# Kernel tuning notes

Hardware: AMD Instinct MI355X
Metric: run time of the kernel (lower is better)

The kernel has to match this reference:

```python
import jax, jax.numpy as jnp
import numpy as np
import math

H = 16
D_MODEL = 1024
D_K = D_MODEL // H


def setup_inputs() -> dict:
    key = jax.random.key(0)
    ks = jax.random.split(key, 11)
    B, S, D = 4, 2048, D_MODEL
    scale = 1.0 / math.sqrt(D)
    inp = {
        "query": jax.random.normal(ks[0], (B, S, D), jnp.float32),
        "key": jax.random.normal(ks[1], (B, S, D), jnp.float32),
        "value": jax.random.normal(ks[2], (B, S, D), jnp.float32),
        # four Linear(d_model, d_model) layers: Wq, Wk, Wv, Wo (weights stored [in, out])
        "Wq": jax.random.normal(ks[3], (D, D), jnp.float32) * scale,
        "bq": jnp.zeros((D,), jnp.float32),
        "Wk": jax.random.normal(ks[4], (D, D), jnp.float32) * scale,
        "bk": jnp.zeros((D,), jnp.float32),
        "Wv": jax.random.normal(ks[5], (D, D), jnp.float32) * scale,
        "bv": jnp.zeros((D,), jnp.float32),
        "Wo": jax.random.normal(ks[6], (D, D), jnp.float32) * scale,
        "bo": jnp.zeros((D,), jnp.float32),
    }
    return inp


def reference(query, key, value, Wq, bq, Wk, bk, Wv, bv, Wo, bo):
    B, S, D = query.shape
    # QKV projections, split into heads: [B, H, S, d_k]
    def proj(x, W, b):
        return (x @ W + b).reshape(B, -1, H, D_K).transpose(0, 2, 1, 3)

    q = proj(query, Wq, bq)
    k = proj(key, Wk, bk)
    v = proj(value, Wv, bv)

    # scaled dot-product attention (mask=None, dropout p=0 -> identity)
    scores = jnp.einsum("bhqd,bhkd->bhqk", q, k) / math.sqrt(D_K)
    p_attn = jax.nn.softmax(scores, axis=-1)
    x = jnp.einsum("bhqk,bhkd->bhqd", p_attn, v)

    # merge heads and output projection
    x = x.transpose(0, 2, 1, 3).reshape(B, -1, H * D_K)
    return x @ Wo + bo
```

## Files before the change

### kernel.cpp

```cpp
#include <hip/hip_runtime.h>


typedef unsigned short u16;
typedef unsigned int u32;
typedef __attribute__((ext_vector_type(8))) short bfx8;
typedef __attribute__((ext_vector_type(4))) float f32x4;
typedef __attribute__((ext_vector_type(16))) float f32x16;
typedef __attribute__((ext_vector_type(4))) float fx4;
typedef __attribute__((ext_vector_type(8))) u16 u16x8;
typedef __attribute__((ext_vector_type(4))) u16 u16x4;
typedef __attribute__((ext_vector_type(4))) u32 u32x4;

__device__ __forceinline__ u16 f2bf(float f) {
  union { float f; u32 u; } v; v.f = f;
  u32 u = v.u;
  u += 0x7fffu + ((u >> 16) & 1u);
  return (u16)(u >> 16);
}

__device__ __forceinline__ u32 cvtpk(float a, float b) {
  u32 r;
  asm("v_cvt_pk_bf16_f32 %0, %1, %2" : "=v"(r) : "v"(a), "v"(b));
  return r;
}

__device__ __forceinline__ void gl_lds16(const void* g, void* l) {
  __builtin_amdgcn_global_load_lds((const __attribute__((address_space(1))) void*)g,
                                   (__attribute__((address_space(3))) void*)l, 16, 0, 0);
}

__global__ void prep(const float* __restrict__ q, const float* __restrict__ k,
                     const float* __restrict__ v, u16* __restrict__ inBase,
                     const float* __restrict__ W0, const float* __restrict__ W1,
                     const float* __restrict__ W2, const float* __restrict__ W3,
                     u16* __restrict__ WtBase) {
  __shared__ float tile[64][65];
  const int bid = blockIdx.x;
  const int t = threadIdx.x;
  if (bid < 12288) {
    const int z = bid >> 12, xb = bid & 4095;
    const float* in = z == 0 ? q : (z == 1 ? k : v);
    u16* out = inBase + (size_t)z * (8192ull * 1024);
    const int i = (xb * 256 + t) * 8;
    fx4 a = *(const fx4*)(in + i);
    fx4 b = *(const fx4*)(in + i + 4);
    u16x8 o;
    o[0] = f2bf(a[0]); o[1] = f2bf(a[1]); o[2] = f2bf(a[2]); o[3] = f2bf(a[3]);
    o[4] = f2bf(b[0]); o[5] = f2bf(b[1]); o[6] = f2bf(b[2]); o[7] = f2bf(b[3]);
    *(u16x8*)(out + i) = o;
  } else {
    const int wb = bid - 12288;
    const int z = wb >> 8, rem = wb & 255;
    const float* W = z == 0 ? W0 : (z == 1 ? W1 : (z == 2 ? W2 : W3));
    u16* Wt = WtBase + (size_t)z * (1024ull * 1024);
    const int n0 = (rem & 15) << 6, k0 = (rem >> 4) << 6;
    {
      int r = t >> 2, c = (t & 3) << 4;
      const float* src = W + (size_t)(k0 + r) * 1024 + n0 + c;
#pragma unroll
      for (int u = 0; u < 4; ++u) {
        fx4 vv = *(const fx4*)(src + u * 4);
        tile[r][c + u * 4 + 0] = vv[0];
        tile[r][c + u * 4 + 1] = vv[1];
        tile[r][c + u * 4 + 2] = vv[2];
        tile[r][c + u * 4 + 3] = vv[3];
      }
    }
    __syncthreads();
    {
      int nn = t >> 2, j = t & 3;
      u16x8 o0, o1;
#pragma unroll
      for (int e = 0; e < 8; ++e) o0[e] = f2bf(tile[(j << 4) + e][nn]);
#pragma unroll
      for (int e = 0; e < 8; ++e) o1[e] = f2bf(tile[(j << 4) + 8 + e][nn]);
      u16* dst = Wt + (size_t)(n0 + nn) * 1024 + k0 + (j << 4);
      *(u16x8*)dst = o0;
      *(u16x8*)(dst + 8) = o1;
    }
  }
}

template <int EPI>
__device__ __forceinline__ void gemm_body(const u16* __restrict__ A, const u16* __restrict__ Bt,
                                          const float* __restrict__ bias, void* __restrict__ out,
                                          float scale, char* smem, int m0, int n0) {
  const int t = threadIdx.x;
  const int w = t >> 6, l = t & 63;
  const int lg = l >> 4, lr = l & 15;
  const int wr = w >> 1, wc = w & 1;

  f32x4 acc[4][4] = {};

  const int trow = t >> 3;
  const int scb = ((t & 7) << 4) ^ ((trow & 7) << 4);
  const char* gA = (const char*)A + (size_t)(m0 + trow) * 2048;
  const char* gB = (const char*)Bt + (size_t)(n0 + trow) * 2048;

#define GSTAGE(kt, buf)                                                        \
  do {                                                                         \
    _Pragma("unroll")                                                          \
    for (int i = 0; i < 4; ++i) {                                              \
      gl_lds16(gA + (size_t)i * 32 * 2048 + ((kt) << 7) + scb,                 \
               (buf) + (((i << 8) + (w << 6)) << 4));                          \
      gl_lds16(gB + (size_t)i * 32 * 2048 + ((kt) << 7) + scb,                 \
               (buf) + 16384 + (((i << 8) + (w << 6)) << 4));                  \
    }                                                                          \
  } while (0)

  GSTAGE(0, smem);
  __syncthreads();

  for (int kt = 0; kt < 16; ++kt) {
    char* sA = smem + ((kt & 1) << 15);
    char* sB = sA + 16384;
    if (kt < 15) GSTAGE(kt + 1, smem + (((kt + 1) & 1) << 15));

#pragma unroll
    for (int kk = 0; kk < 2; ++kk) {
      const int off = ((kk << 6) + (lg << 4)) ^ ((lr & 7) << 4);
      bfx8 av[4], bv[4];
#pragma unroll
      for (int fi = 0; fi < 4; ++fi)
        av[fi] = *(const bfx8*)(sA + ((wr << 6) + (fi << 4) + lr) * 128 + off);
#pragma unroll
      for (int fj = 0; fj < 4; ++fj)
        bv[fj] = *(const bfx8*)(sB + ((wc << 6) + (fj << 4) + lr) * 128 + off);
#pragma unroll
      for (int fi = 0; fi < 4; ++fi)
#pragma unroll
        for (int fj = 0; fj < 4; ++fj)
          acc[fi][fj] = __builtin_amdgcn_mfma_f32_16x16x32_bf16(av[fi], bv[fj], acc[fi][fj], 0, 0, 0);
    }
    __syncthreads();
  }
#undef GSTAGE

#pragma unroll
  for (int fj = 0; fj < 4; ++fj) {
    const int n = n0 + (wc << 6) + (fj << 4) + lr;
    const float bvl = bias[n];
#pragma unroll
    for (int fi = 0; fi < 4; ++fi) {
      if constexpr (EPI == 2) {
        const int h = n >> 6, d = n & 63;
        const int mm = m0 + (wr << 6) + (fi << 4) + (lg << 2);
        const int b = mm >> 11, s = mm & 2047;
        u16x4 pk4;
#pragma unroll
        for (int r = 0; r < 4; ++r) pk4[r] = f2bf(acc[fi][fj][r] + bvl);
        *(u16x4*)((u16*)out + (size_t)(b * 16 + h) * 131072 + (size_t)d * 2048 + s) = pk4;
      } else {
#pragma unroll
        for (int r = 0; r < 4; ++r) {
          const int m = m0 + (wr << 6) + (fi << 4) + (lg << 2) + r;
          const float val = (acc[fi][fj][r] + bvl) * scale;
          if constexpr (EPI == 0) {
            const int b = m >> 11, s = m & 2047, h = n >> 6, d = n & 63;
            ((u16*)out)[(((size_t)(b * 16 + h) * 2048 + s) << 6) + d] = f2bf(val);
          } else {
            ((float*)out)[((size_t)m << 10) + n] = val;
          }
        }
      }
    }
  }
}

__device__ __forceinline__ void xcd_remap(int& m0, int& n0) {
  const int lin = blockIdx.x + (blockIdx.y << 3);
  const int c = lin & 7, j = lin >> 3;
  m0 = (((j & 7) << 3) + c) << 7;
  n0 = (j >> 3) << 7;
}

__global__ void __launch_bounds__(256, 2)
gemm_qkv(const u16* __restrict__ A0, const u16* __restrict__ Wt0,
         const float* __restrict__ bq, const float* __restrict__ bk,
         const float* __restrict__ bv, u16* __restrict__ out0, u16* __restrict__ vt) {
  __shared__ __align__(16) char smem[65536];
  const int z = blockIdx.z;
  int m0, n0;
  xcd_remap(m0, n0);
  const u16* A = A0 + (size_t)z * (8192ull * 1024);
  const u16* Bt = Wt0 + (size_t)z * (1024ull * 1024);
  if (z == 2) {
    gemm_body<2>(A, Bt, bv, vt, 1.0f, smem, m0, n0);
  } else {
    const float* bias = z == 0 ? bq : bk;
    const float scale = z == 0 ? 0.18033688011112042f : 1.0f;
    gemm_body<0>(A, Bt, bias, out0 + (size_t)z * (8192ull * 1024), scale, smem, m0, n0);
  }
}

__global__ void __launch_bounds__(256, 2)
gemm_o(const u16* __restrict__ A, const u16* __restrict__ Bt,
       const float* __restrict__ bias, float* __restrict__ out) {
  __shared__ __align__(16) char smem[65536];
  int m0, n0;
  xcd_remap(m0, n0);
  gemm_body<1>(A, Bt, bias, out, 1.0f, smem, m0, n0);
}

__global__ void __launch_bounds__(512, 4)
attn_fwd(const u16* __restrict__ Qg, const u16* __restrict__ Kg,
         const u16* __restrict__ Vtg, u16* __restrict__ Og) {
  __shared__ __align__(16) char smem[65536];
  const int t = threadIdx.x;
  const int w = t >> 6, l = t & 63;
  const int l31 = l & 31, hi = l >> 5;

  const int id = blockIdx.x;
  const int xcd = id & 7, slot = id >> 3;
  const int pair = ((slot >> 3) << 3) + xcd;
  const int q0 = (slot & 7) << 8;

  const char* Qb = (const char*)Qg + ((size_t)pair << 18);
  const char* Kb = (const char*)Kg + ((size_t)pair << 18);
  const char* Vb = (const char*)Vtg + ((size_t)pair << 18);

  const int trow = t >> 3;
  const int scb = (((t & 7) ^ (trow & 7) ^ (((trow >> 3) & 3) << 1)) << 4);
  const int ldst = (w << 10);
  const int swz = (((l & 7) ^ ((l31 >> 3) << 1)) << 4);

  bfx8 qf[4];
#pragma unroll
  for (int ks = 0; ks < 4; ++ks)
    qf[ks] = *(const bfx8*)(Qb + (size_t)(q0 + (w << 5) + l31) * 128 + (ks << 5) + (hi << 4));

  f32x16 accO[2] = {};
  float Lp = 0.f;

#define ASTAGE(kt, buf)                                                         \
  do {                                                                          \
    gl_lds16(Kb + (size_t)(kt) * 8192 + (size_t)trow * 128 + scb, (buf) + ldst);\
    gl_lds16(Vb + (size_t)trow * 4096 + (size_t)(kt) * 128 + scb,               \
             (buf) + 8192 + ldst);                                              \
  } while (0)

  ASTAGE(0, smem);
  ASTAGE(1, smem + 16384);
  __syncthreads();

  for (int it2 = 0; it2 < 16; ++it2) {
    const int tt = it2 << 1;
    if (tt + 2 < 32) ASTAGE(tt + 2, smem + (((tt + 2) & 3) << 14));
    if (tt + 3 < 32) ASTAGE(tt + 3, smem + (((tt + 3) & 3) << 14));

#pragma unroll
    for (int u = 0; u < 2; ++u) {
      char* bK = smem + (((tt + u) & 3) << 14);
      char* bV = bK + 8192;

      f32x16 accS[2] = {{}, {}};
      __builtin_amdgcn_s_setprio(1);
#pragma unroll
      for (int mb = 0; mb < 2; ++mb) {
        bfx8 kf[4];
#pragma unroll
        for (int ks = 0; ks < 4; ++ks)
          kf[ks] = *(const bfx8*)(bK + (((mb << 5) + l31) << 7) + (((ks << 5) + (hi << 4)) ^ swz));
#pragma unroll
        for (int ks = 0; ks < 4; ++ks)
          accS[mb] = __builtin_amdgcn_mfma_f32_32x32x16_bf16(kf[ks], qf[ks], accS[mb], 0, 0, 0);
      }
      __builtin_amdgcn_s_setprio(0);

      bfx8 pa[4];
#pragma unroll
      for (int mb = 0; mb < 2; ++mb) {
#pragma unroll
        for (int r = 0; r < 16; ++r) {
          accS[mb][r] = __builtin_amdgcn_exp2f(accS[mb][r]);
          Lp += accS[mb][r];
        }
#pragma unroll
        for (int half = 0; half < 2; ++half) {
          u32 a0 = cvtpk(accS[mb][8 * half + 0], accS[mb][8 * half + 1]);
          u32 a1 = cvtpk(accS[mb][8 * half + 2], accS[mb][8 * half + 3]);
          u32 b0 = cvtpk(accS[mb][8 * half + 4], accS[mb][8 * half + 5]);
          u32 b1 = cvtpk(accS[mb][8 * half + 6], accS[mb][8 * half + 7]);
          asm volatile("v_permlane32_swap_b32 %0, %1" : "+v"(a0), "+v"(b0));
          asm volatile("v_permlane32_swap_b32 %0, %1" : "+v"(a1), "+v"(b1));
          u32x4 pk; pk[0] = a0; pk[1] = a1; pk[2] = b0; pk[3] = b1;
          pa[(mb << 1) + half] = *(bfx8*)&pk;
        }
      }

      __builtin_amdgcn_s_setprio(1);
#pragma unroll
      for (int ks = 0; ks < 4; ++ks) {
        bfx8 vf0 = *(const bfx8*)(bV + ((0 + l31) << 7) + (((ks << 5) + (hi << 4)) ^ swz));
        bfx8 vf1 = *(const bfx8*)(bV + ((32 + l31) << 7) + (((ks << 5) + (hi << 4)) ^ swz));
        accO[0] = __builtin_amdgcn_mfma_f32_32x32x16_bf16(pa[ks], vf0, accO[0], 0, 0, 0);
        accO[1] = __builtin_amdgcn_mfma_f32_32x32x16_bf16(pa[ks], vf1, accO[1], 0, 0, 0);
      }
      __builtin_amdgcn_s_setprio(0);
    }

    __syncthreads();
  }
#undef ASTAGE

  const float Ltot = Lp + __shfl_xor(Lp, 32);
  const int b = pair >> 4, h = pair & 15;
  u16* dstBase = Og + (((size_t)(b * 2048 + q0 + (w << 5))) << 10) + (h << 6) + l31;
#pragma unroll
  for (int r = 0; r < 16; ++r) {
    const int ql = (r & 3) + ((r >> 2) << 3) + (hi << 2);
    const float Lr = __shfl(Ltot, ql);
    const float rinv = __builtin_amdgcn_rcpf(Lr);
    u16* dst = dstBase + ((size_t)ql << 10);
    dst[0]  = f2bf(accO[0][r] * rinv);
    dst[32] = f2bf(accO[1][r] * rinv);
  }
}

extern "C" void kernel_launch(void* const* d_in, const int* in_sizes, int n_in,
                              void* d_out, int out_size, void* d_ws, size_t ws_size,
                              hipStream_t stream) {
  const float* q  = (const float*)d_in[0];
  const float* k  = (const float*)d_in[1];
  const float* v  = (const float*)d_in[2];
  const float* Wq = (const float*)d_in[3];
  const float* bq = (const float*)d_in[4];
  const float* Wk = (const float*)d_in[5];
  const float* bk = (const float*)d_in[6];
  const float* Wv = (const float*)d_in[7];
  const float* bv = (const float*)d_in[8];
  const float* Wo = (const float*)d_in[9];
  const float* bo = (const float*)d_in[10];
  float* out = (float*)d_out;
  char* ws = (char*)d_ws;

  const size_t MB = 1024 * 1024;
  if (ws_size < 104 * MB) return;

  u16* inq = (u16*)(ws + 0 * MB);
  u16* wqt = (u16*)(ws + 48 * MB);
  u16* wot = (u16*)(ws + 54 * MB);
  u16* Qh  = (u16*)(ws + 56 * MB);
  u16* Kh  = (u16*)(ws + 72 * MB);
  u16* Vth = (u16*)(ws + 88 * MB);
  u16* Ob  = inq;

  prep<<<13312, 256, 0, stream>>>(q, k, v, inq, Wq, Wk, Wv, Wo, wqt);
  gemm_qkv<<<dim3(8, 64, 3), 256, 0, stream>>>(inq, wqt, bq, bk, bv, Qh, Vth);
  attn_fwd<<<512, 512, 0, stream>>>(Qh, Kh, Vth, Ob);
  gemm_o<<<dim3(8, 64), 256, 0, stream>>>(Ob, wot, bo, out);
}
```

Baseline: 182.4 us.

## Process two query groups per warp in attention to reuse K/V tiles

Each attention warp now handles 64 query rows (two 32-row groups) instead of 32, so every block covers 512 queries and the grid halves to 256 blocks. K and V fragments loaded from LDS are reused across both query groups, halving K/V global and LDS traffic per query. The cost is more registers (launch bounds relaxed to 2 blocks/CU), fewer blocks on a 256-CU part, and less latency hiding. A local rename of bv in the GEMM is cosmetic.

```diff
diff --git a/kernel.cpp b/kernel.cpp
--- a/kernel.cpp
+++ b/kernel.cpp
@@ -119,18 +119,18 @@
 #pragma unroll
     for (int kk = 0; kk < 2; ++kk) {
       const int off = ((kk << 6) + (lg << 4)) ^ ((lr & 7) << 4);
-      bfx8 av[4], bv[4];
+      bfx8 av[4], bv4[4];
 #pragma unroll
       for (int fi = 0; fi < 4; ++fi)
         av[fi] = *(const bfx8*)(sA + ((wr << 6) + (fi << 4) + lr) * 128 + off);
 #pragma unroll
       for (int fj = 0; fj < 4; ++fj)
-        bv[fj] = *(const bfx8*)(sB + ((wc << 6) + (fj << 4) + lr) * 128 + off);
+        bv4[fj] = *(const bfx8*)(sB + ((wc << 6) + (fj << 4) + lr) * 128 + off);
 #pragma unroll
       for (int fi = 0; fi < 4; ++fi)
 #pragma unroll
         for (int fj = 0; fj < 4; ++fj)
-          acc[fi][fj] = __builtin_amdgcn_mfma_f32_16x16x32_bf16(av[fi], bv[fj], acc[fi][fj], 0, 0, 0);
+          acc[fi][fj] = __builtin_amdgcn_mfma_f32_16x16x32_bf16(av[fi], bv4[fj], acc[fi][fj], 0, 0, 0);
     }
     __syncthreads();
   }
@@ -202,7 +202,7 @@
   gemm_body<1>(A, Bt, bias, out, 1.0f, smem, m0, n0);
 }
 
-__global__ void __launch_bounds__(512, 4)
+__global__ void __launch_bounds__(512, 2)
 attn_fwd(const u16* __restrict__ Qg, const u16* __restrict__ Kg,
          const u16* __restrict__ Vtg, u16* __restrict__ Og) {
   __shared__ __align__(16) char smem[65536];
@@ -212,8 +212,8 @@
 
   const int id = blockIdx.x;
   const int xcd = id & 7, slot = id >> 3;
-  const int pair = ((slot >> 3) << 3) + xcd;
-  const int q0 = (slot & 7) << 8;
+  const int pair = ((slot >> 2) << 3) + xcd;
+  const int q0 = (slot & 3) << 9;
 
   const char* Qb = (const char*)Qg + ((size_t)pair << 18);
   const char* Kb = (const char*)Kg + ((size_t)pair << 18);
@@ -224,13 +224,16 @@
   const int ldst = (w << 10);
   const int swz = (((l & 7) ^ ((l31 >> 3) << 1)) << 4);
 
-  bfx8 qf[4];
-#pragma unroll
-  for (int ks = 0; ks < 4; ++ks)
-    qf[ks] = *(const bfx8*)(Qb + (size_t)(q0 + (w << 5) + l31) * 128 + (ks << 5) + (hi << 4));
-
-  f32x16 accO[2] = {};
-  float Lp = 0.f;
+  bfx8 qf[2][4];
+#pragma unroll
+  for (int qg = 0; qg < 2; ++qg)
+#pragma unroll
+    for (int ks = 0; ks < 4; ++ks)
+      qf[qg][ks] = *(const bfx8*)(Qb + (size_t)(q0 + (w << 6) + (qg << 5) + l31) * 128 +
+                                  (ks << 5) + (hi << 4));
+
+  f32x16 accO[2][2] = {};
+  float Lp[2] = {0.f, 0.f};
 
 #define ASTAGE(kt, buf)                                                         \
   do {                                                                          \
@@ -253,8 +256,7 @@
       char* bK = smem + (((tt + u) & 3) << 14);
       char* bV = bK + 8192;
 
-      f32x16 accS[2] = {{}, {}};
-      __builtin_amdgcn_s_setprio(1);
+      bfx8 pa[2][4];
 #pragma unroll
       for (int mb = 0; mb < 2; ++mb) {
         bfx8 kf[4];
@@ -262,29 +264,29 @@
         for (int ks = 0; ks < 4; ++ks)
           kf[ks] = *(const bfx8*)(bK + (((mb << 5) + l31) << 7) + (((ks << 5) + (hi << 4)) ^ swz));
 #pragma unroll
-        for (int ks = 0; ks < 4; ++ks)
-          accS[mb] = __builtin_amdgcn_mfma_f32_32x32x16_bf16(kf[ks], qf[ks], accS[mb], 0, 0, 0);
-      }
-      __builtin_amdgcn_s_setprio(0);
-
-      bfx8 pa[4];
-#pragma unroll
-      for (int mb = 0; mb < 2; ++mb) {
-#pragma unroll
-        for (int r = 0; r < 16; ++r) {
-          accS[mb][r] = __builtin_amdgcn_exp2f(accS[mb][r]);
-          Lp += accS[mb][r];
-        }
-#pragma unroll
-        for (int half = 0; half < 2; ++half) {
-          u32 a0 = cvtpk(accS[mb][8 * half + 0], accS[mb][8 * half + 1]);
-          u32 a1 = cvtpk(accS[mb][8 * half + 2], accS[mb][8 * half + 3]);
-          u32 b0 = cvtpk(accS[mb][8 * half + 4], accS[mb][8 * half + 5]);
-          u32 b1 = cvtpk(accS[mb][8 * half + 6], accS[mb][8 * half + 7]);
-          asm volatile("v_permlane32_swap_b32 %0, %1" : "+v"(a0), "+v"(b0));
-          asm volatile("v_permlane32_swap_b32 %0, %1" : "+v"(a1), "+v"(b1));
-          u32x4 pk; pk[0] = a0; pk[1] = a1; pk[2] = b0; pk[3] = b1;
-          pa[(mb << 1) + half] = *(bfx8*)&pk;
+        for (int qg = 0; qg < 2; ++qg) {
+          f32x16 accS = {};
+          __builtin_amdgcn_s_setprio(1);
+#pragma unroll
+          for (int ks = 0; ks < 4; ++ks)
+            accS = __builtin_amdgcn_mfma_f32_32x32x16_bf16(kf[ks], qf[qg][ks], accS, 0, 0, 0);
+          __builtin_amdgcn_s_setprio(0);
+#pragma unroll
+          for (int r = 0; r < 16; ++r) {
+            accS[r] = __builtin_amdgcn_exp2f(accS[r]);
+            Lp[qg] += accS[r];
+          }
+#pragma unroll
+          for (int half = 0; half < 2; ++half) {
+            u32 a0 = cvtpk(accS[8 * half + 0], accS[8 * half + 1]);
+            u32 a1 = cvtpk(accS[8 * half + 2], accS[8 * half + 3]);
+            u32 b0 = cvtpk(accS[8 * half + 4], accS[8 * half + 5]);
+            u32 b1 = cvtpk(accS[8 * half + 6], accS[8 * half + 7]);
+            asm volatile("v_permlane32_swap_b32 %0, %1" : "+v"(a0), "+v"(b0));
+            asm volatile("v_permlane32_swap_b32 %0, %1" : "+v"(a1), "+v"(b1));
+            u32x4 pk; pk[0] = a0; pk[1] = a1; pk[2] = b0; pk[3] = b1;
+            pa[qg][(mb << 1) + half] = *(bfx8*)&pk;
+          }
         }
       }
 
@@ -293,8 +295,11 @@
       for (int ks = 0; ks < 4; ++ks) {
         bfx8 vf0 = *(const bfx8*)(bV + ((0 + l31) << 7) + (((ks << 5) + (hi << 4)) ^ swz));
         bfx8 vf1 = *(const bfx8*)(bV + ((32 + l31) << 7) + (((ks << 5) + (hi << 4)) ^ swz));
-        accO[0] = __builtin_amdgcn_mfma_f32_32x32x16_bf16(pa[ks], vf0, accO[0], 0, 0, 0);
-        accO[1] = __builtin_amdgcn_mfma_f32_32x32x16_bf16(pa[ks], vf1, accO[1], 0, 0, 0);
+#pragma unroll
+        for (int qg = 0; qg < 2; ++qg) {
+          accO[qg][0] = __builtin_amdgcn_mfma_f32_32x32x16_bf16(pa[qg][ks], vf0, accO[qg][0], 0, 0, 0);
+          accO[qg][1] = __builtin_amdgcn_mfma_f32_32x32x16_bf16(pa[qg][ks], vf1, accO[qg][1], 0, 0, 0);
+        }
       }
       __builtin_amdgcn_s_setprio(0);
     }
@@ -303,17 +308,20 @@
   }
 #undef ASTAGE
 
-  const float Ltot = Lp + __shfl_xor(Lp, 32);
   const int b = pair >> 4, h = pair & 15;
-  u16* dstBase = Og + (((size_t)(b * 2048 + q0 + (w << 5))) << 10) + (h << 6) + l31;
-#pragma unroll
-  for (int r = 0; r < 16; ++r) {
-    const int ql = (r & 3) + ((r >> 2) << 3) + (hi << 2);
-    const float Lr = __shfl(Ltot, ql);
-    const float rinv = __builtin_amdgcn_rcpf(Lr);
-    u16* dst = dstBase + ((size_t)ql << 10);
-    dst[0]  = f2bf(accO[0][r] * rinv);
-    dst[32] = f2bf(accO[1][r] * rinv);
+#pragma unroll
+  for (int qg = 0; qg < 2; ++qg) {
+    const float Ltot = Lp[qg] + __shfl_xor(Lp[qg], 32);
+    u16* dstBase = Og + (((size_t)(b * 2048 + q0 + (w << 6) + (qg << 5))) << 10) + (h << 6) + l31;
+#pragma unroll
+    for (int r = 0; r < 16; ++r) {
+      const int ql = (r & 3) + ((r >> 2) << 3) + (hi << 2);
+      const float Lr = __shfl(Ltot, ql);
+      const float rinv = __builtin_amdgcn_rcpf(Lr);
+      u16* dst = dstBase + ((size_t)ql << 10);
+      dst[0]  = f2bf(accO[qg][0][r] * rinv);
+      dst[32] = f2bf(accO[qg][1][r] * rinv);
+    }
   }
 }
 
@@ -347,6 +355,6 @@
 
   prep<<<13312, 256, 0, stream>>>(q, k, v, inq, Wq, Wk, Wv, Wo, wqt);
   gemm_qkv<<<dim3(8, 64, 3), 256, 0, stream>>>(inq, wqt, bq, bk, bv, Qh, Vth);
-  attn_fwd<<<512, 512, 0, stream>>>(Qh, Kh, Vth, Ob);
+  attn_fwd<<<256, 512, 0, stream>>>(Qh, Kh, Vth, Ob);
   gemm_o<<<dim3(8, 64), 256, 0, stream>>>(Ob, wot, bo, out);
 }
```

Result: slower. 188.1 us (+3.1%).
